# Optimization experiments

Measured on AMD Instinct MI355X. Metric: run time of the kernel, lower is better.

The kernel has to match this reference:

```python
import jax, jax.numpy as jnp
import numpy as np
from jax.scipy.special import logsumexp

SIGMA = 1.0
EPSILON = 1.0
MAX_ITER = 10


def _gaussian_kernel(x, y, sigma):
    # x: (b, l, d), y: (b, k, d) -> (b, l, k) negative-kernel matrix exp(-||x-y||^2 / (2 sigma^2))
    outer = jnp.einsum('bld,bkd->blk', x, y)
    norm_x = jnp.sum(x * x, axis=2)
    norm_y = jnp.sum(y * y, axis=2)
    dist = (norm_x[:, :, None] + norm_y[:, None, :] - 2.0 * outer) / (2.0 * sigma ** 2)
    return jnp.exp(-jnp.maximum(dist, 0.0))


def setup_inputs() -> dict:
    key = jax.random.key(0)
    kx, ka, ky, kb = jax.random.split(key, 4)
    B, L, K, D = 8, 2048, 2048, 32
    return {
        'x': jax.random.normal(kx, (B, L, D), dtype=jnp.float32),
        'a': jax.random.normal(ka, (B, L), dtype=jnp.float32),
        'y': jax.random.normal(ky, (B, K, D), dtype=jnp.float32),
        'b': jax.random.normal(kb, (B, K), dtype=jnp.float32),
    }


def _sinkhorn_potentials(x, a, y, b):
    sg = jax.lax.stop_gradient
    # Kernel matrices (carry gradient wrt x, y); weights a, b are detached inside kernels.
    Kxx = _gaussian_kernel(x, x, SIGMA) / EPSILON + sg(a)[:, None, :]
    Kyx_base = _gaussian_kernel(y, x, SIGMA)
    Kyx = Kyx_base / EPSILON + sg(a)[:, None, :]
    Kxy = jnp.swapaxes(Kyx_base, 1, 2) / EPSILON + sg(b)[:, None, :]
    Kyy = _gaussian_kernel(y, y, SIGMA) / EPSILON + sg(b)[:, None, :]

    # Sinkhorn loop runs under no_grad in the original: stop-gradient kernels.
    Kxx_s, Kyx_s, Kxy_s, Kyy_s = sg(Kxx), sg(Kyx), sg(Kxy), sg(Kyy)

    def step(carry, _):
        fxx, fyx, fxy, fyy = carry
        # sequential (Gauss-Seidel) update order matches the torch dict order xx, yx, xy, yy
        fxx = 0.5 * fxx - 0.5 * logsumexp(Kxx_s + fxx[:, None, :], axis=2)
        fyx = 0.5 * fyx - 0.5 * logsumexp(Kyx_s + fxy[:, None, :], axis=2)  # uses old fxy
        fxy = 0.5 * fxy - 0.5 * logsumexp(Kxy_s + fyx[:, None, :], axis=2)  # uses new fyx
        fyy = 0.5 * fyy - 0.5 * logsumexp(Kyy_s + fyy[:, None, :], axis=2)
        return (fxx, fyx, fxy, fyy), None

    init = (jnp.zeros_like(a), jnp.zeros_like(b), jnp.zeros_like(a), jnp.zeros_like(b))
    (fxx, fyx, fxy, fyy), _ = jax.lax.scan(step, init, None, length=MAX_ITER)

    # Final differentiable extrapolation step (potentials are detached constants).
    fe_xx = -logsumexp(Kxx + fxx[:, None, :], axis=2)
    fe_yx = -logsumexp(Kyx + fxy[:, None, :], axis=2)
    fe_xy = -logsumexp(Kxy + fyx[:, None, :], axis=2)
    fe_yy = -logsumexp(Kyy + fyy[:, None, :], axis=2)
    f = fe_xy - fe_xx  # (b, l)
    g = fe_yx - fe_yy  # (b, k)
    return f, g


def reference(x, a, y, b):
    f, g = _sinkhorn_potentials(x, a, y, b)
    res = jnp.sum(f * jnp.exp(a), axis=1) + jnp.sum(g * jnp.exp(b), axis=1)
    return res * EPSILON  # (batch,)
```

## Files before the change

kernel.cpp:

```cpp
#include <hip/hip_runtime.h>
#include <hip/hip_bf16.h>

#define B_ 8
#define N_ 2048
#define D_ 32
#define RCAP 16
#define EM1_DIAG 1.7182818284590452f
#define M_   8.0f
#define EM_  2980.9579870417283f

typedef __attribute__((ext_vector_type(8))) short short8;
typedef __attribute__((ext_vector_type(4))) float f32x4;

__global__ void setup_kernel(const float* __restrict__ x, const float* __restrict__ y,
                             unsigned short* __restrict__ xb, unsigned short* __restrict__ yb,
                             float* __restrict__ NX, float* __restrict__ NY,
                             int* __restrict__ csr_cnt)
{
    int t = blockIdx.x * 256 + threadIdx.x;
    const float* src = (t < 16384) ? x : y;
    unsigned short* dstb = (t < 16384) ? xb : yb;
    float* dstn = (t < 16384) ? NX : NY;
    int row = (t < 16384) ? t : (t - 16384);
    const float4* p = reinterpret_cast<const float4*>(src + (size_t)row * D_);
    float ss = 0.f;
    float4 v[8];
    #pragma unroll
    for (int k = 0; k < 8; k++) {
        v[k] = p[k];
        ss += v[k].x * v[k].x + v[k].y * v[k].y + v[k].z * v[k].z + v[k].w * v[k].w;
    }
    short8* dst8 = reinterpret_cast<short8*>(dstb + (size_t)row * D_);
    #pragma unroll
    for (int k = 0; k < 4; k++) {
        const float fv[8] = { v[2*k].x, v[2*k].y, v[2*k].z, v[2*k].w,
                              v[2*k+1].x, v[2*k+1].y, v[2*k+1].z, v[2*k+1].w };
        short8 o;
        #pragma unroll
        for (int e = 0; e < 8; e++) {
            __hip_bfloat16 h = __float2bfloat16(fv[e]);
            o[e] = *reinterpret_cast<const short*>(&h);
        }
        dst8[k] = o;
    }
    dstn[row] = ss * 0.5f;
    csr_cnt[2 * t] = 0;
    csr_cnt[2 * t + 1] = 0;
}

__global__ __launch_bounds__(256) void discover_kernel(
    const unsigned short* __restrict__ xb, const unsigned short* __restrict__ yb,
    const float* __restrict__ NX, const float* __restrict__ NY,
    int* __restrict__ csr_cnt, uint2* __restrict__ csr_ent)
{
    int m = blockIdx.x >> 8;
    int rem = blockIdx.x & 255;
    int batch = rem >> 5;
    int rowblk = rem & 31;
    const unsigned short* rd = (m == 0) ? xb : yb;
    const float*          rN = (m == 0) ? NX : NY;
    const unsigned short* cd = (m == 1) ? yb : xb;
    const float*          cN = (m == 1) ? NY : NX;

    const int tid = threadIdx.x, lane = tid & 63, wv = tid >> 6;
    const int r0 = rowblk * 64;
    const size_t rowbase = (size_t)batch * N_ + r0;

    short8 afrag[4];
    f32x4 cinit[4];
    #pragma unroll
    for (int g = 0; g < 4; g++) {
        afrag[g] = *reinterpret_cast<const short8*>(
            rd + (rowbase + g * 16 + (lane & 15)) * D_ + (lane >> 4) * 8);
        float4 nv = *reinterpret_cast<const float4*>(
            rN + rowbase + g * 16 + (lane >> 4) * 4);
        cinit[g][0] = -nv.x; cinit[g][1] = -nv.y; cinit[g][2] = -nv.z; cinit[g][3] = -nv.w;
    }
    const unsigned short* cdB = cd + (size_t)batch * N_ * D_;
    const float* cNB = cN + batch * N_;
    const int c0w = wv * 512;

    unsigned mask = 0;
    #pragma unroll 8
    for (int cc = 0; cc < 32; ++cc) {
        int col = c0w + cc * 16 + (lane & 15);
        short8 bfrag = *reinterpret_cast<const short8*>(
            cdB + (size_t)col * D_ + (lane >> 4) * 8);
        float ny = cNB[col];
        f32x4 d[4];
        #pragma unroll
        for (int g = 0; g < 4; g++)
            d[g] = __builtin_amdgcn_mfma_f32_16x16x32_bf16(afrag[g], bfrag, cinit[g], 0, 0, 0);
        float m0 = fmaxf(fmaxf(d[0][0], d[0][1]), fmaxf(d[0][2], d[0][3]));
        float m1 = fmaxf(fmaxf(d[1][0], d[1][1]), fmaxf(d[1][2], d[1][3]));
        float m2 = fmaxf(fmaxf(d[2][0], d[2][1]), fmaxf(d[2][2], d[2][3]));
        float m3 = fmaxf(fmaxf(d[3][0], d[3][1]), fmaxf(d[3][2], d[3][3]));
        float mx = fmaxf(fmaxf(m0, m1), fmaxf(m2, m3));
        mask |= (__any(mx > ny - 10.0f) ? 1u : 0u) << cc;
    }

    auto push = [&](int T, int row, int colv, float em1) {
        size_t base = (size_t)(T * B_ + batch) * N_ + row;
        int idx = atomicAdd(&csr_cnt[base], 1);
        if (idx < RCAP)
            csr_ent[base * RCAP + idx] = make_uint2((unsigned)colv, __float_as_uint(em1));
    };
    while (mask) {
        int cc = __builtin_ctz(mask);
        mask &= mask - 1;
        int col = c0w + cc * 16 + (lane & 15);
        short8 bfrag = *reinterpret_cast<const short8*>(
            cdB + (size_t)col * D_ + (lane >> 4) * 8);
        float ny = cNB[col];
        f32x4 d[4];
        #pragma unroll
        for (int g = 0; g < 4; g++)
            d[g] = __builtin_amdgcn_mfma_f32_16x16x32_bf16(afrag[g], bfrag, cinit[g], 0, 0, 0);
        #pragma unroll
        for (int g = 0; g < 4; g++) {
            #pragma unroll
            for (int r = 0; r < 4; r++) {
                float dist = ny - d[g][r];
                if (dist < 10.0f) {
                    int i = r0 + g * 16 + (lane >> 4) * 4 + r;
                    if (m == 2) {
                        float em1 = __expf(__expf(-fmaxf(dist, 0.f))) - 1.0f;
                        push(2, i, col, em1);
                        push(3, col, i, em1);
                    } else if (i != col) {
                        float em1 = __expf(__expf(-fmaxf(dist, 0.f))) - 1.0f;
                        push(m, i, col, em1);
                    }
                }
            }
        }
    }
}

__device__ __forceinline__ float tree8(const float* r) {
    return ((r[0] + r[1]) + (r[2] + r[3])) + ((r[4] + r[5]) + (r[6] + r[7]));
}

__global__ __launch_bounds__(512) void sinkhorn_kernel(
    const float* __restrict__ a_in, const float* __restrict__ b_in,
    const int* __restrict__ csr_cnt, const uint2* __restrict__ csr_ent,
    float* __restrict__ out)
{
    __shared__ float f[4][N_];
    __shared__ float ew[2][N_];
    __shared__ float evb[2][4][N_];
    __shared__ float red2[2][4][8];
    __shared__ float resacc;

    const int batch = blockIdx.x;
    const int t = threadIdx.x, lane = t & 63, wv = t >> 6;

    int cnts[4][4];
    const uint2* ebase[4];
    #pragma unroll
    for (int T = 0; T < 4; T++) {
        size_t bb = (size_t)(T * B_ + batch) * N_;
        ebase[T] = csr_ent + bb * RCAP;
        #pragma unroll
        for (int q = 0; q < 4; q++)
            cnts[T][q] = min(csr_cnt[bb + t + 512 * q], RCAP);
    }
    #pragma unroll
    for (int q = 0; q < 4; q++) {
        int j = t + 512 * q;
        ew[0][j] = __expf(a_in[batch * N_ + j] - M_);
        ew[1][j] = __expf(b_in[batch * N_ + j] - M_);
        f[0][j] = 0.f; f[1][j] = 0.f; f[2][j] = 0.f; f[3][j] = 0.f;
    }
    if (t == 0) resacc = 0.f;

    auto gath = [&](const uint2* E, int cnt, const float* evbuf) -> float {
        float g = 0.f;
        for (int k = 0; k < cnt; ++k) {
            uint2 e = E[k];
            g += evbuf[e.x] * __uint_as_float(e.y);
        }
        return g;
    };
    auto wred = [&](float& s) {
        #pragma unroll
        for (int off = 1; off < 64; off <<= 1) s += __shfl_xor(s, off, 64);
    };

    auto stageA = [&](int par) {
        float s0 = 0.f, s1 = 0.f, s2 = 0.f;
        float e0q[4], e2q[4], f0o[4], f1o[4], f3o[4];
        #pragma unroll
        for (int q = 0; q < 4; q++) {
            int j = t + 512 * q;
            f0o[q] = f[0][j]; f1o[q] = f[1][j]; float f2v = f[2][j]; f3o[q] = f[3][j];
            float e0 = ew[0][j] * __expf(f0o[q]); evb[par][0][j] = e0; e0q[q] = e0; s0 += e0;
            float e1 = ew[0][j] * __expf(f2v);    evb[par][1][j] = e1;              s1 += e1;
            float e2 = ew[1][j] * __expf(f3o[q]); evb[par][2][j] = e2; e2q[q] = e2; s2 += e2;
        }
        wred(s0); wred(s1); wred(s2);
        if (lane == 0) { red2[par][0][wv] = s0; red2[par][1][wv] = s1; red2[par][2][wv] = s2; }
        __syncthreads();
        float S0 = tree8(red2[par][0]), S1 = tree8(red2[par][1]), S2 = tree8(red2[par][2]);
        #pragma unroll
        for (int q = 0; q < 4; q++) {
            int i = t + 512 * q;
            float g0 = gath(ebase[0] + (size_t)i * RCAP, cnts[0][q], evb[par][0]);
            f[0][i] = 0.5f * f0o[q] - 0.5f * (M_ + __logf(S0 + e0q[q] * EM1_DIAG + g0));
            float g1 = gath(ebase[2] + (size_t)i * RCAP, cnts[2][q], evb[par][1]);
            f[1][i] = 0.5f * f1o[q] - 0.5f * (M_ + __logf(S1 + g1));
            float g2 = gath(ebase[1] + (size_t)i * RCAP, cnts[1][q], evb[par][2]);
            f[3][i] = 0.5f * f3o[q] - 0.5f * (M_ + __logf(S2 + e2q[q] * EM1_DIAG + g2));
        }
    };

    auto stageB = [&](int par) {
        float sB = 0.f;
        float f2o[4];
        #pragma unroll
        for (int q = 0; q < 4; q++) {
            int j = t + 512 * q;
            f2o[q] = f[2][j];
            float ee = ew[1][j] * __expf(f[1][j]); evb[par][0][j] = ee; sB += ee;
        }
        wred(sB);
        if (lane == 0) red2[par][0][wv] = sB;
        __syncthreads();
        float S = tree8(red2[par][0]);
        #pragma unroll
        for (int q = 0; q < 4; q++) {
            int i = t + 512 * q;
            float g = gath(ebase[3] + (size_t)i * RCAP, cnts[3][q], evb[par][0]);
            f[2][i] = 0.5f * f2o[q] - 0.5f * (M_ + __logf(S + g));
        }
    };

    int s = 0;
    for (int it = 0; it < 10; ++it) {
        stageA(s & 1); s++;
        stageB(s & 1); s++;
    }

    {
        int par = s & 1;
        float s0 = 0.f, s1 = 0.f, s2 = 0.f, s3 = 0.f;
        float e0q[4], e3q[4];
        #pragma unroll
        for (int q = 0; q < 4; q++) {
            int j = t + 512 * q;
            float e0 = ew[0][j] * __expf(f[0][j]); evb[par][0][j] = e0; e0q[q] = e0; s0 += e0;
            float e1 = ew[0][j] * __expf(f[2][j]); evb[par][1][j] = e1;              s1 += e1;
            float e2 = ew[1][j] * __expf(f[1][j]); evb[par][2][j] = e2;              s2 += e2;
            float e3 = ew[1][j] * __expf(f[3][j]); evb[par][3][j] = e3; e3q[q] = e3; s3 += e3;
        }
        wred(s0); wred(s1); wred(s2); wred(s3);
        if (lane == 0) { red2[par][0][wv] = s0; red2[par][1][wv] = s1;
                         red2[par][2][wv] = s2; red2[par][3][wv] = s3; }
        __syncthreads();
        float S0 = tree8(red2[par][0]), S1 = tree8(red2[par][1]);
        float S2 = tree8(red2[par][2]), S3 = tree8(red2[par][3]);
        float ctr = 0.f;
        #pragma unroll
        for (int q = 0; q < 4; q++) {
            int i = t + 512 * q;
            float r0 = M_ + __logf(S0 + e0q[q] * EM1_DIAG +
                                   gath(ebase[0] + (size_t)i * RCAP, cnts[0][q], evb[par][0]));
            float r1 = M_ + __logf(S1 + gath(ebase[2] + (size_t)i * RCAP, cnts[2][q], evb[par][1]));
            float r2 = M_ + __logf(S2 + gath(ebase[3] + (size_t)i * RCAP, cnts[3][q], evb[par][2]));
            float r3 = M_ + __logf(S3 + e3q[q] * EM1_DIAG +
                                   gath(ebase[1] + (size_t)i * RCAP, cnts[1][q], evb[par][3]));
            ctr += (r0 - r2) * ew[0][i] * EM_ + (r3 - r1) * ew[1][i] * EM_;
        }
        wred(ctr);
        if (lane == 0) atomicAdd(&resacc, ctr);
        __syncthreads();
        if (t == 0) out[batch] = resacc;
    }
}

extern "C" void kernel_launch(void* const* d_in, const int* in_sizes, int n_in,
                              void* d_out, int out_size, void* d_ws, size_t ws_size,
                              hipStream_t stream)
{
    const float* x = (const float*)d_in[0];
    const float* a = (const float*)d_in[1];
    const float* y = (const float*)d_in[2];
    const float* b = (const float*)d_in[3];
    float* out = (float*)d_out;

    char* ws = (char*)d_ws;
    size_t o = 0;
    unsigned short* xb = (unsigned short*)(ws + o); o += (size_t)B_ * N_ * D_ * 2;
    unsigned short* yb = (unsigned short*)(ws + o); o += (size_t)B_ * N_ * D_ * 2;
    float* NX = (float*)(ws + o); o += (size_t)B_ * N_ * 4;
    float* NY = (float*)(ws + o); o += (size_t)B_ * N_ * 4;
    int* csr_cnt = (int*)(ws + o); o += (size_t)4 * B_ * N_ * 4;
    uint2* csr_ent = (uint2*)(ws + o); o += (size_t)4 * B_ * N_ * RCAP * 8;

    setup_kernel<<<128, 256, 0, stream>>>(x, y, xb, yb, NX, NY, csr_cnt);
    discover_kernel<<<3 * 256, 256, 0, stream>>>(xb, yb, NX, NY, csr_cnt, csr_ent);
    sinkhorn_kernel<<<B_, 512, 0, stream>>>(a, b, csr_cnt, csr_ent, out);
}
```

Before: 207.7 us.

## Keep Sinkhorn potentials in registers, use 1024 threads and atomic block sums

The sinkhorn kernel now runs 1024 threads per batch block and keeps the potentials and log-weights in registers instead of shared arrays. Per-wave partial sums are combined with shared-memory atomics into a triple-buffered accumulator, replacing the per-wave reduction table and tree sum. Exp and log are done in base 2 through AMD intrinsics with FMAs. The goal is fewer shared-memory loads and stores and more parallelism in this serial, latency-bound phase. The cost is more register pressure per thread and float atomic ordering that is not deterministic.

Result: faster. 168.3 us (-19.0%).

```diff
diff --git a/kernel.cpp b/kernel.cpp
--- a/kernel.cpp
+++ b/kernel.cpp
@@ -8,6 +8,9 @@
 #define EM1_DIAG 1.7182818284590452f
 #define M_   8.0f
 #define EM_  2980.9579870417283f
+#define L2E  1.4426950408889634f
+#define LN2  0.6931471805599453f
+#define MH_  (0.5f * M_ * L2E)
 
 typedef __attribute__((ext_vector_type(8))) short short8;
 typedef __attribute__((ext_vector_type(4))) float f32x4;
@@ -137,42 +140,38 @@
     }
 }
 
-__device__ __forceinline__ float tree8(const float* r) {
-    return ((r[0] + r[1]) + (r[2] + r[3])) + ((r[4] + r[5]) + (r[6] + r[7]));
-}
-
-__global__ __launch_bounds__(512) void sinkhorn_kernel(
+__global__ __launch_bounds__(1024) void sinkhorn_kernel(
     const float* __restrict__ a_in, const float* __restrict__ b_in,
     const int* __restrict__ csr_cnt, const uint2* __restrict__ csr_ent,
     float* __restrict__ out)
 {
-    __shared__ float f[4][N_];
-    __shared__ float ew[2][N_];
     __shared__ float evb[2][4][N_];
-    __shared__ float red2[2][4][8];
+    __shared__ float Sacc[3][4];
     __shared__ float resacc;
 
     const int batch = blockIdx.x;
-    const int t = threadIdx.x, lane = t & 63, wv = t >> 6;
-
-    int cnts[4][4];
+    const int t = threadIdx.x, lane = t & 63;
+
+    int cnts[4][2];
     const uint2* ebase[4];
     #pragma unroll
     for (int T = 0; T < 4; T++) {
         size_t bb = (size_t)(T * B_ + batch) * N_;
-        ebase[T] = csr_ent + bb * RCAP;
-        #pragma unroll
-        for (int q = 0; q < 4; q++)
-            cnts[T][q] = min(csr_cnt[bb + t + 512 * q], RCAP);
-    }
-    #pragma unroll
-    for (int q = 0; q < 4; q++) {
-        int j = t + 512 * q;
-        ew[0][j] = __expf(a_in[batch * N_ + j] - M_);
-        ew[1][j] = __expf(b_in[batch * N_ + j] - M_);
-        f[0][j] = 0.f; f[1][j] = 0.f; f[2][j] = 0.f; f[3][j] = 0.f;
-    }
+        ebase[T] = csr_ent + bb * (size_t)RCAP;
+        cnts[T][0] = min(csr_cnt[bb + t], RCAP);
+        cnts[T][1] = min(csr_cnt[bb + t + 1024], RCAP);
+    }
+    float AW[2], BW[2];
+    float F0[2] = {0.f, 0.f}, F1[2] = {0.f, 0.f}, F2[2] = {0.f, 0.f}, F3[2] = {0.f, 0.f};
+    #pragma unroll
+    for (int q = 0; q < 2; q++) {
+        int j = t + 1024 * q;
+        AW[q] = (a_in[batch * N_ + j] - M_) * L2E;
+        BW[q] = (b_in[batch * N_ + j] - M_) * L2E;
+    }
+    if (t < 12) (&Sacc[0][0])[t] = 0.f;
     if (t == 0) resacc = 0.f;
+    __syncthreads();
 
     auto gath = [&](const uint2* E, int cnt, const float* evbuf) -> float {
         float g = 0.f;
@@ -182,96 +181,107 @@
         }
         return g;
     };
-    auto wred = [&](float& s) {
-        #pragma unroll
-        for (int off = 1; off < 64; off <<= 1) s += __shfl_xor(s, off, 64);
-    };
-
-    auto stageA = [&](int par) {
+    auto wredadd = [&](float v, float* dst) {
+        #pragma unroll
+        for (int off = 1; off < 64; off <<= 1) v += __shfl_xor(v, off, 64);
+        if (lane == 0) atomicAdd(dst, v);
+    };
+
+    auto stageA = [&](int s) {
+        const int p2 = s & 1, p3 = s % 3, p3n = (s + 1) % 3;
+        float e0q[2], e2q[2];
         float s0 = 0.f, s1 = 0.f, s2 = 0.f;
-        float e0q[4], e2q[4], f0o[4], f1o[4], f3o[4];
-        #pragma unroll
-        for (int q = 0; q < 4; q++) {
-            int j = t + 512 * q;
-            f0o[q] = f[0][j]; f1o[q] = f[1][j]; float f2v = f[2][j]; f3o[q] = f[3][j];
-            float e0 = ew[0][j] * __expf(f0o[q]); evb[par][0][j] = e0; e0q[q] = e0; s0 += e0;
-            float e1 = ew[0][j] * __expf(f2v);    evb[par][1][j] = e1;              s1 += e1;
-            float e2 = ew[1][j] * __expf(f3o[q]); evb[par][2][j] = e2; e2q[q] = e2; s2 += e2;
-        }
-        wred(s0); wred(s1); wred(s2);
-        if (lane == 0) { red2[par][0][wv] = s0; red2[par][1][wv] = s1; red2[par][2][wv] = s2; }
+        #pragma unroll
+        for (int q = 0; q < 2; q++) {
+            int j = t + 1024 * q;
+            float e0 = __builtin_amdgcn_exp2f(AW[q] + F0[q]); evb[p2][0][j] = e0; e0q[q] = e0; s0 += e0;
+            float e1 = __builtin_amdgcn_exp2f(AW[q] + F2[q]); evb[p2][1][j] = e1;              s1 += e1;
+            float e2 = __builtin_amdgcn_exp2f(BW[q] + F3[q]); evb[p2][2][j] = e2; e2q[q] = e2; s2 += e2;
+        }
+        wredadd(s0, &Sacc[p3][0]);
+        wredadd(s1, &Sacc[p3][1]);
+        wredadd(s2, &Sacc[p3][2]);
+        if (t == 0) { Sacc[p3n][0] = 0.f; Sacc[p3n][1] = 0.f; Sacc[p3n][2] = 0.f; Sacc[p3n][3] = 0.f; }
         __syncthreads();
-        float S0 = tree8(red2[par][0]), S1 = tree8(red2[par][1]), S2 = tree8(red2[par][2]);
-        #pragma unroll
-        for (int q = 0; q < 4; q++) {
-            int i = t + 512 * q;
-            float g0 = gath(ebase[0] + (size_t)i * RCAP, cnts[0][q], evb[par][0]);
-            f[0][i] = 0.5f * f0o[q] - 0.5f * (M_ + __logf(S0 + e0q[q] * EM1_DIAG + g0));
-            float g1 = gath(ebase[2] + (size_t)i * RCAP, cnts[2][q], evb[par][1]);
-            f[1][i] = 0.5f * f1o[q] - 0.5f * (M_ + __logf(S1 + g1));
-            float g2 = gath(ebase[1] + (size_t)i * RCAP, cnts[1][q], evb[par][2]);
-            f[3][i] = 0.5f * f3o[q] - 0.5f * (M_ + __logf(S2 + e2q[q] * EM1_DIAG + g2));
-        }
-    };
-
-    auto stageB = [&](int par) {
+        float S0 = Sacc[p3][0], S1 = Sacc[p3][1], S2 = Sacc[p3][2];
+        #pragma unroll
+        for (int q = 0; q < 2; q++) {
+            int i = t + 1024 * q;
+            float g0 = gath(ebase[0] + (size_t)i * RCAP, cnts[0][q], evb[p2][0]);
+            float g1 = gath(ebase[2] + (size_t)i * RCAP, cnts[2][q], evb[p2][1]);
+            float g2 = gath(ebase[1] + (size_t)i * RCAP, cnts[1][q], evb[p2][2]);
+            float lg0 = __builtin_amdgcn_logf(S0 + fmaf(e0q[q], EM1_DIAG, g0));
+            float lg1 = __builtin_amdgcn_logf(S1 + g1);
+            float lg2 = __builtin_amdgcn_logf(S2 + fmaf(e2q[q], EM1_DIAG, g2));
+            F0[q] = fmaf(0.5f, F0[q], -fmaf(0.5f, lg0, MH_));
+            F1[q] = fmaf(0.5f, F1[q], -fmaf(0.5f, lg1, MH_));
+            F3[q] = fmaf(0.5f, F3[q], -fmaf(0.5f, lg2, MH_));
+        }
+    };
+
+    auto stageB = [&](int s) {
+        const int p2 = s & 1, p3 = s % 3, p3n = (s + 1) % 3;
         float sB = 0.f;
-        float f2o[4];
-        #pragma unroll
-        for (int q = 0; q < 4; q++) {
-            int j = t + 512 * q;
-            f2o[q] = f[2][j];
-            float ee = ew[1][j] * __expf(f[1][j]); evb[par][0][j] = ee; sB += ee;
-        }
-        wred(sB);
-        if (lane == 0) red2[par][0][wv] = sB;
+        #pragma unroll
+        for (int q = 0; q < 2; q++) {
+            int j = t + 1024 * q;
+            float e = __builtin_amdgcn_exp2f(BW[q] + F1[q]); evb[p2][0][j] = e; sB += e;
+        }
+        wredadd(sB, &Sacc[p3][0]);
+        if (t == 0) { Sacc[p3n][0] = 0.f; Sacc[p3n][1] = 0.f; Sacc[p3n][2] = 0.f; Sacc[p3n][3] = 0.f; }
         __syncthreads();
-        float S = tree8(red2[par][0]);
-        #pragma unroll
-        for (int q = 0; q < 4; q++) {
-            int i = t + 512 * q;
-            float g = gath(ebase[3] + (size_t)i * RCAP, cnts[3][q], evb[par][0]);
-            f[2][i] = 0.5f * f2o[q] - 0.5f * (M_ + __logf(S + g));
+        float S = Sacc[p3][0];
+        #pragma unroll
+        for (int q = 0; q < 2; q++) {
+            int i = t + 1024 * q;
+            float g = gath(ebase[3] + (size_t)i * RCAP, cnts[3][q], evb[p2][0]);
+            F2[q] = fmaf(0.5f, F2[q], -fmaf(0.5f, __builtin_amdgcn_logf(S + g), MH_));
         }
     };
 
     int s = 0;
     for (int it = 0; it < 10; ++it) {
-        stageA(s & 1); s++;
-        stageB(s & 1); s++;
+        stageA(s); ++s;
+        stageB(s); ++s;
     }
 
     {
-        int par = s & 1;
+        const int p2 = s & 1, p3 = s % 3;
+        float e0q[2], e3q[2];
         float s0 = 0.f, s1 = 0.f, s2 = 0.f, s3 = 0.f;
-        float e0q[4], e3q[4];
-        #pragma unroll
-        for (int q = 0; q < 4; q++) {
-            int j = t + 512 * q;
-            float e0 = ew[0][j] * __expf(f[0][j]); evb[par][0][j] = e0; e0q[q] = e0; s0 += e0;
-            float e1 = ew[0][j] * __expf(f[2][j]); evb[par][1][j] = e1;              s1 += e1;
-            float e2 = ew[1][j] * __expf(f[1][j]); evb[par][2][j] = e2;              s2 += e2;
-            float e3 = ew[1][j] * __expf(f[3][j]); evb[par][3][j] = e3; e3q[q] = e3; s3 += e3;
-        }
-        wred(s0); wred(s1); wred(s2); wred(s3);
-        if (lane == 0) { red2[par][0][wv] = s0; red2[par][1][wv] = s1;
-                         red2[par][2][wv] = s2; red2[par][3][wv] = s3; }
+        #pragma unroll
+        for (int q = 0; q < 2; q++) {
+            int j = t + 1024 * q;
+            float e0 = __builtin_amdgcn_exp2f(AW[q] + F0[q]); evb[p2][0][j] = e0; e0q[q] = e0; s0 += e0;
+            float e1 = __builtin_amdgcn_exp2f(AW[q] + F2[q]); evb[p2][1][j] = e1;              s1 += e1;
+            float e2 = __builtin_amdgcn_exp2f(BW[q] + F1[q]); evb[p2][2][j] = e2;              s2 += e2;
+            float e3 = __builtin_amdgcn_exp2f(BW[q] + F3[q]); evb[p2][3][j] = e3; e3q[q] = e3; s3 += e3;
+        }
+        wredadd(s0, &Sacc[p3][0]);
+        wredadd(s1, &Sacc[p3][1]);
+        wredadd(s2, &Sacc[p3][2]);
+        wredadd(s3, &Sacc[p3][3]);
         __syncthreads();
-        float S0 = tree8(red2[par][0]), S1 = tree8(red2[par][1]);
-        float S2 = tree8(red2[par][2]), S3 = tree8(red2[par][3]);
+        float S0 = Sacc[p3][0], S1 = Sacc[p3][1], S2 = Sacc[p3][2], S3 = Sacc[p3][3];
         float ctr = 0.f;
         #pragma unroll
-        for (int q = 0; q < 4; q++) {
-            int i = t + 512 * q;
-            float r0 = M_ + __logf(S0 + e0q[q] * EM1_DIAG +
-                                   gath(ebase[0] + (size_t)i * RCAP, cnts[0][q], evb[par][0]));
-            float r1 = M_ + __logf(S1 + gath(ebase[2] + (size_t)i * RCAP, cnts[2][q], evb[par][1]));
-            float r2 = M_ + __logf(S2 + gath(ebase[3] + (size_t)i * RCAP, cnts[3][q], evb[par][2]));
-            float r3 = M_ + __logf(S3 + e3q[q] * EM1_DIAG +
-                                   gath(ebase[1] + (size_t)i * RCAP, cnts[1][q], evb[par][3]));
-            ctr += (r0 - r2) * ew[0][i] * EM_ + (r3 - r1) * ew[1][i] * EM_;
-        }
-        wred(ctr);
+        for (int q = 0; q < 2; q++) {
+            int i = t + 1024 * q;
+            float lg0 = __builtin_amdgcn_logf(S0 + fmaf(e0q[q], EM1_DIAG,
+                            gath(ebase[0] + (size_t)i * RCAP, cnts[0][q], evb[p2][0])));
+            float lg1 = __builtin_amdgcn_logf(S1 +
+                            gath(ebase[2] + (size_t)i * RCAP, cnts[2][q], evb[p2][1]));
+            float lg2 = __builtin_amdgcn_logf(S2 +
+                            gath(ebase[3] + (size_t)i * RCAP, cnts[3][q], evb[p2][2]));
+            float lg3 = __builtin_amdgcn_logf(S3 + fmaf(e3q[q], EM1_DIAG,
+                            gath(ebase[1] + (size_t)i * RCAP, cnts[1][q], evb[p2][3])));
+            float ea = __builtin_amdgcn_exp2f(AW[q]);
+            float eb = __builtin_amdgcn_exp2f(BW[q]);
+            ctr += (lg0 - lg2) * ea + (lg3 - lg1) * eb;
+        }
+        ctr *= (LN2 * EM_);
+        #pragma unroll
+        for (int off = 1; off < 64; off <<= 1) ctr += __shfl_xor(ctr, off, 64);
         if (lane == 0) atomicAdd(&resacc, ctr);
         __syncthreads();
         if (t == 0) out[batch] = resacc;
@@ -299,5 +309,5 @@
 
     setup_kernel<<<128, 256, 0, stream>>>(x, y, xb, yb, NX, NY, csr_cnt);
     discover_kernel<<<3 * 256, 256, 0, stream>>>(xb, yb, NX, NY, csr_cnt, csr_ent);
-    sinkhorn_kernel<<<B_, 512, 0, stream>>>(a, b, csr_cnt, csr_ent, out);
+    sinkhorn_kernel<<<B_, 1024, 0, stream>>>(a, b, csr_cnt, csr_ent, out);
 }
```
